# Optimization experiments

Hardware: AMD Instinct MI355X
Metric: run time of the kernel (lower is better)

Reference implementation:

```python
import jax, jax.numpy as jnp
import numpy as np

NUM_GROUPS = 8   # num_groups1, recursive_index=False path
NUM_HEADS = 8


def setup_inputs() -> dict:
    key = jax.random.key(0)
    k1, k2, k3 = jax.random.split(key, 3)
    B, C, H, W = 4, 256, 64, 64
    x = jax.random.normal(k1, (B, C, H, W), dtype=jnp.float32)
    w_qkv = jax.random.normal(k2, (3 * C, C), dtype=jnp.float32) * 0.02
    w_proj = jax.random.normal(k3, (C, C), dtype=jnp.float32) * 0.02
    b_proj = jnp.zeros((C,), dtype=jnp.float32)
    return {"x": x, "w_qkv": w_qkv, "w_proj": w_proj, "b_proj": b_proj}


def reference(x, w_qkv, w_proj, b_proj):
    B, C, H, W = x.shape
    N = H * W
    G = NUM_GROUPS
    nh = NUM_HEADS
    hd = C // nh
    M = N // G
    scale = hd ** -0.5

    # b c h w -> b (h w) c
    xf = x.reshape(B, C, N).transpose(0, 2, 1)  # [B, N, C]

    # qkv linear (no bias), then split into groups / heads
    qkv = (xf @ w_qkv.T).reshape(B, G, M, 3, nh, hd)
    qkv = jnp.transpose(qkv, (3, 0, 1, 4, 2, 5))  # [3, B, G, nh, M, hd]
    q, k, v = qkv[0], qkv[1], qkv[2]

    # grouped multi-head attention, manual softmax
    attn = jax.nn.softmax(jnp.einsum('bghmd,bghnd->bghmn', q, k) * scale, axis=-1)
    out = jnp.einsum('bghmn,bghnd->bghmd', attn, v)

    # [B,G,nh,M,hd] -> [B,G,M,C] -> [B,N,C]
    out = out.transpose(0, 1, 3, 2, 4).reshape(B, N, C)

    out = out @ w_proj.T + b_proj

    # b (h w) c -> b c h w
    return out.transpose(0, 2, 1).reshape(B, C, H, W)
```

## Files before the change

kernel.cpp:

```cpp
#include <hip/hip_runtime.h>
#include <hip/hip_bf16.h>

#define Bb 4
#define Cc 256
#define Nn 4096
#define Gg 8
#define NHh 8
#define HDd 32
#define Mm 512

typedef __bf16 bf16_t;
typedef __bf16 bf16x2 __attribute__((ext_vector_type(2)));
typedef __bf16 bf16x4 __attribute__((ext_vector_type(4)));
typedef __bf16 bf16x8 __attribute__((ext_vector_type(8)));
typedef float f32x4 __attribute__((ext_vector_type(4)));

#define LSCALE (0.17677669529663687f * 1.44269504088896340f)

__device__ __forceinline__ void load_lds16(const bf16_t* g, bf16_t* l) {
  __builtin_amdgcn_global_load_lds(
      (const __attribute__((address_space(1))) void*)g,
      (__attribute__((address_space(3))) void*)l, 16, 0, 0);
}

__global__ __launch_bounds__(256) void prep_kernel(
    const float* __restrict__ x, bf16_t* __restrict__ xT,
    const float* __restrict__ wqkv, const float* __restrict__ wproj,
    bf16_t* __restrict__ wq_b, bf16_t* __restrict__ wp_b) {
  int bid = blockIdx.x, tid = threadIdx.x;
  if (bid >= 1024) {
    int i = (bid - 1024) * 256 + tid;
    wq_b[i] = (bf16_t)wqkv[i];
    if (i < Cc * Cc) wp_b[i] = (bf16_t)wproj[i];
    return;
  }
  __shared__ float t[64][65];
  int b = bid >> 8, c0 = ((bid >> 6) & 3) * 64, n0 = (bid & 63) * 64;
  const float* xp = x + ((long long)b * Cc + c0) * Nn + n0;
#pragma unroll
  for (int it = 0; it < 4; ++it) {
    int idx = it * 256 + tid;
    int r = idx >> 4, col = (idx & 15) * 4;
    f32x4 v = *(const f32x4*)&xp[(long long)r * Nn + col];
    t[r][col] = v[0];
    t[r][col + 1] = v[1];
    t[r][col + 2] = v[2];
    t[r][col + 3] = v[3];
  }
  __syncthreads();
  bf16_t* op = xT + ((long long)b * Nn + n0) * Cc + c0;
#pragma unroll
  for (int it = 0; it < 2; ++it) {
    int idx = it * 256 + tid;
    int n = idx >> 3, cg = (idx & 7) * 8;
    bf16x8 w;
#pragma unroll
    for (int j = 0; j < 8; ++j) w[j] = (bf16_t)t[cg + j][n];
    *(bf16x8*)&op[(long long)n * Cc + cg] = w;
  }
}

__global__ __launch_bounds__(256, 4) void qkv_gemm_kernel(
    const bf16_t* __restrict__ xT, const bf16_t* __restrict__ wqb,
    bf16_t* __restrict__ Qh, bf16_t* __restrict__ Kh, bf16_t* __restrict__ Vh) {
  __shared__ bf16_t smem[20480];
  int bid = blockIdx.x;
  int m0 = (bid / 3) * 64;
  int n0 = (bid % 3) * 256;
  int tid = threadIdx.x, lane = tid & 63, wid = tid >> 6;
  int quad = lane >> 4, l16 = lane & 15;
  int wn = wid * 64;

  f32x4 acc[4][4];
#pragma unroll
  for (int i = 0; i < 4; ++i)
#pragma unroll
    for (int j = 0; j < 4; ++j) acc[i][j] = (f32x4){0.f, 0.f, 0.f, 0.f};

  int scol = (lane & 3) * 8;
  int arow = lane >> 2;
  auto stage = [&](int bufi, int k0) {
    load_lds16(&xT[(long long)(m0 + wid * 16 + arow) * Cc + k0 + scol],
               &smem[bufi * 2048 + wid * 512]);
#pragma unroll
    for (int r = 0; r < 4; ++r) {
      int ch = wid * 4 + r;
      load_lds16(&wqb[(long long)(n0 + ch * 16 + arow) * Cc + k0 + scol],
                 &smem[4096 + bufi * 8192 + ch * 512]);
    }
  };

  stage(0, 0);
  __syncthreads();
  for (int t = 0; t < 8; ++t) {
    if (t < 7) stage((t + 1) & 1, (t + 1) * 32);
    const bf16_t* Ap = &smem[(t & 1) * 2048];
    const bf16_t* Bp = &smem[4096 + (t & 1) * 8192];
    bf16x8 a[4], b[4];
#pragma unroll
    for (int i = 0; i < 4; ++i)
      a[i] = *(const bf16x8*)&Ap[(i * 16 + l16) * 32 + quad * 8];
#pragma unroll
    for (int j = 0; j < 4; ++j)
      b[j] = *(const bf16x8*)&Bp[(wn + j * 16 + l16) * 32 + quad * 8];
#pragma unroll
    for (int i = 0; i < 4; ++i)
#pragma unroll
      for (int j = 0; j < 4; ++j)
        acc[i][j] = __builtin_amdgcn_mfma_f32_16x16x32_bf16(a[i], b[j], acc[i][j], 0, 0, 0);
    __syncthreads();
  }

  if (n0 < 512) {
    const bool isQ = (n0 == 0);
    const float s = isQ ? LSCALE : 1.0f;
#pragma unroll
    for (int i = 0; i < 4; ++i)
#pragma unroll
      for (int j = 0; j < 4; ++j) {
        int f = wn + j * 16 + l16;
#pragma unroll
        for (int r = 0; r < 4; ++r) {
          int lm = i * 16 + quad * 4 + r;
          smem[lm * 268 + f] = (bf16_t)(acc[i][j][r] * s);
        }
      }
    __syncthreads();
    int lm = tid >> 2, d0 = (tid & 3) * 8;
    int row = m0 + lm;
    int bb = row >> 12, gg = (row >> 9) & 7, m = row & 511;
    bf16_t* dst = isQ ? Qh : Kh;
#pragma unroll
    for (int hh = 0; hh < 8; ++hh) {
      long long hb = (long long)((bb << 6) | (gg << 3) | hh) * (Mm * HDd);
      bf16x8 w = *(bf16x8*)&smem[lm * 268 + hh * 32 + d0];
      *(bf16x8*)&dst[hb + m * HDd + d0] = w;
    }
  } else {
#pragma unroll
    for (int i = 0; i < 4; ++i)
#pragma unroll
      for (int j = 0; j < 4; ++j) {
        int f = wn + j * 16 + l16;
#pragma unroll
        for (int r = 0; r < 4; ++r)
          smem[f * 72 + i * 16 + quad * 4 + r] = (bf16_t)acc[i][j][r];
      }
    __syncthreads();
    int bb = m0 >> 12, gg = (m0 >> 9) & 7, mb = m0 & 511;
#pragma unroll
    for (int it = 0; it < 8; ++it) {
      int idx = it * 256 + tid;
      int f = idx >> 3, seg = idx & 7;
      int hh = f >> 5, d = f & 31;
      long long hb = (long long)((bb << 6) | (gg << 3) | hh) * (Mm * HDd);
      bf16x8 w = *(bf16x8*)&smem[f * 72 + seg * 8];
      *(bf16x8*)&Vh[hb + (long long)d * Mm + mb + seg * 8] = w;
    }
  }
}

__global__ __launch_bounds__(256, 4) void attn_kernel(
    const bf16_t* __restrict__ Qh, const bf16_t* __restrict__ Kh,
    const bf16_t* __restrict__ Vh, bf16_t* __restrict__ Oa) {
  __shared__ bf16_t Ks[256 * 32];
  __shared__ bf16_t Vs[32 * 264];
  int gid = blockIdx.x;
  int ms = gid & 3, head = gid >> 2;
  int h = head & 7, g = (head >> 3) & 7, b = head >> 6;
  int tid = threadIdx.x, lane = tid & 63, wid = tid >> 6;
  int quad = lane >> 4, l16 = lane & 15;

  const bf16_t* Kg = Kh + (long long)head * (Mm * HDd);
  const bf16_t* Vg = Vh + (long long)head * (Mm * HDd);
  const bf16_t* Qg = Qh + (long long)head * (Mm * HDd) + (ms * 128 + wid * 32) * HDd;

  bf16x8 qa = *(const bf16x8*)&Qg[l16 * HDd + quad * 8];
  bf16x8 qb = *(const bf16x8*)&Qg[(16 + l16) * HDd + quad * 8];

  bf16x8 ones;
#pragma unroll
  for (int i = 0; i < 8; ++i) ones[i] = (bf16_t)1.0f;

  int rp0 = ((l16 >> 2) << 3) | (l16 & 3);
  const bf16_t* Kp0 = &Ks[rp0 * HDd + quad * 8];
  const bf16_t* Kp1 = Kp0 + 4 * HDd;
  const bf16_t* VsL = &Vs[l16 * 264 + quad * 8];
  const bf16_t* VsH = &Vs[(16 + l16) * 264 + quad * 8];
  const f32x4 zero = (f32x4){0.f, 0.f, 0.f, 0.f};

  f32x4 oLa = zero, oHa = zero, oLb = zero, oHb = zero;
  f32x4 ra = zero, rb = zero;

  auto inner = [&]() {
#pragma unroll
    for (int c = 0; c < 8; ++c) {
      int nb = c * 32;
      bf16x8 kf0 = *(const bf16x8*)&Kp0[nb * HDd];
      bf16x8 kf1 = *(const bf16x8*)&Kp1[nb * HDd];
      f32x4 sa0 = __builtin_amdgcn_mfma_f32_16x16x32_bf16(kf0, qa, zero, 0, 0, 0);
      f32x4 sa1 = __builtin_amdgcn_mfma_f32_16x16x32_bf16(kf1, qa, zero, 0, 0, 0);
      f32x4 sb0 = __builtin_amdgcn_mfma_f32_16x16x32_bf16(kf0, qb, zero, 0, 0, 0);
      f32x4 sb1 = __builtin_amdgcn_mfma_f32_16x16x32_bf16(kf1, qb, zero, 0, 0, 0);
      bf16x8 pa, pb;
#pragma unroll
      for (int r = 0; r < 4; ++r) {
        pa[r] = (bf16_t)__builtin_exp2f(sa0[r]);
        pa[4 + r] = (bf16_t)__builtin_exp2f(sa1[r]);
        pb[r] = (bf16_t)__builtin_exp2f(sb0[r]);
        pb[4 + r] = (bf16_t)__builtin_exp2f(sb1[r]);
      }
      bf16x8 vL = *(const bf16x8*)&VsL[nb];
      bf16x8 vH = *(const bf16x8*)&VsH[nb];
      oLa = __builtin_amdgcn_mfma_f32_16x16x32_bf16(vL, pa, oLa, 0, 0, 0);
      oHa = __builtin_amdgcn_mfma_f32_16x16x32_bf16(vH, pa, oHa, 0, 0, 0);
      oLb = __builtin_amdgcn_mfma_f32_16x16x32_bf16(vL, pb, oLb, 0, 0, 0);
      oHb = __builtin_amdgcn_mfma_f32_16x16x32_bf16(vH, pb, oHb, 0, 0, 0);
      ra = __builtin_amdgcn_mfma_f32_16x16x32_bf16(ones, pa, ra, 0, 0, 0);
      rb = __builtin_amdgcn_mfma_f32_16x16x32_bf16(ones, pb, rb, 0, 0, 0);
    }
  };

#pragma unroll
  for (int it = 0; it < 4; ++it) {
    int ch = wid * 4 + it;
    load_lds16(&Kg[ch * 512 + lane * 8], &Ks[ch * 512]);
  }
  bf16x8 vcur[4], vnxt[4];
#pragma unroll
  for (int i = 0; i < 4; ++i) {
    int idx = i * 256 + tid;
    int d = idx >> 5, c16 = idx & 31;
    vcur[i] = *(const bf16x8*)&Vg[d * Mm + c16 * 8];
    vnxt[i] = *(const bf16x8*)&Vg[d * Mm + 256 + c16 * 8];
  }
#pragma unroll
  for (int i = 0; i < 4; ++i) {
    int idx = i * 256 + tid;
    int d = idx >> 5, c16 = idx & 31;
    *(bf16x8*)&Vs[d * 264 + c16 * 8] = vcur[i];
  }
  __syncthreads();
  inner();
  __syncthreads();
#pragma unroll
  for (int it = 0; it < 4; ++it) {
    int ch = wid * 4 + it;
    load_lds16(&Kg[8192 + ch * 512 + lane * 8], &Ks[ch * 512]);
  }
#pragma unroll
  for (int i = 0; i < 4; ++i) {
    int idx = i * 256 + tid;
    int d = idx >> 5, c16 = idx & 31;
    *(bf16x8*)&Vs[d * 264 + c16 * 8] = vnxt[i];
  }
  __syncthreads();
  inner();

  float inva = 1.f / ra[0], invb = 1.f / rb[0];

  long long orowa =
      ((long long)(b * Nn + g * Mm + ms * 128 + wid * 32 + l16)) * Cc + h * HDd;
  long long orowb = orowa + 16 * Cc;
  bf16x4 wLa, wHa, wLb, wHb;
#pragma unroll
  for (int r = 0; r < 4; ++r) {
    wLa[r] = (bf16_t)(oLa[r] * inva);
    wHa[r] = (bf16_t)(oHa[r] * inva);
    wLb[r] = (bf16_t)(oLb[r] * invb);
    wHb[r] = (bf16_t)(oHb[r] * invb);
  }
  *(bf16x4*)&Oa[orowa + quad * 4] = wLa;
  *(bf16x4*)&Oa[orowa + 16 + quad * 4] = wHa;
  *(bf16x4*)&Oa[orowb + quad * 4] = wLb;
  *(bf16x4*)&Oa[orowb + 16 + quad * 4] = wHb;
}

__global__ __launch_bounds__(256, 4) void proj_kernel(
    const bf16_t* __restrict__ Wp, const bf16_t* __restrict__ Oa,
    float* __restrict__ out, const float* __restrict__ bias) {
  __shared__ bf16_t As[2][64 * 32];
  __shared__ bf16_t Bs[2][64 * 32];
  int tid = threadIdx.x, lane = tid & 63, wid = tid >> 6;
  int quad = lane >> 4, l16 = lane & 15;
  int z = blockIdx.z;
  const bf16_t* Bt = Oa + (long long)z * Nn * Cc;
  int m0 = blockIdx.y * 64, n0 = blockIdx.x * 64;

  f32x4 acc[4];
#pragma unroll
  for (int i = 0; i < 4; ++i) acc[i] = (f32x4){0.f, 0.f, 0.f, 0.f};

  int scol = (lane & 3) * 8;
  int arow = lane >> 2;
  auto stage = [&](int bufi, int k0) {
    load_lds16(&Wp[(long long)(m0 + wid * 16 + arow) * Cc + k0 + scol],
               &As[bufi][wid * 512]);
    load_lds16(&Bt[(long long)(n0 + wid * 16 + arow) * Cc + k0 + scol],
               &Bs[bufi][wid * 512]);
  };

  stage(0, 0);
  __syncthreads();
  for (int t = 0; t < 8; ++t) {
    if (t < 7) stage((t + 1) & 1, (t + 1) * 32);
    const bf16_t* Ap = As[t & 1];
    const bf16_t* Bp = Bs[t & 1];
    bf16x8 a[4], b;
#pragma unroll
    for (int i = 0; i < 4; ++i)
      a[i] = *(const bf16x8*)&Ap[(i * 16 + l16) * 32 + quad * 8];
    b = *(const bf16x8*)&Bp[(wid * 16 + l16) * 32 + quad * 8];
#pragma unroll
    for (int i = 0; i < 4; ++i)
      acc[i] = __builtin_amdgcn_mfma_f32_16x16x32_bf16(a[i], b, acc[i], 0, 0, 0);
    __syncthreads();
  }

#pragma unroll
  for (int i = 0; i < 4; ++i) {
    int col = n0 + wid * 16 + l16;
#pragma unroll
    for (int r = 0; r < 4; ++r) {
      int row = m0 + i * 16 + quad * 4 + r;
      out[(long long)z * (Cc * Nn) + (long long)row * Nn + col] =
          acc[i][r] + bias[row];
    }
  }
}

extern "C" void kernel_launch(void* const* d_in, const int* in_sizes, int n_in,
                              void* d_out, int out_size, void* d_ws, size_t ws_size,
                              hipStream_t stream) {
  (void)in_sizes; (void)n_in; (void)out_size; (void)ws_size;
  const float* x = (const float*)d_in[0];
  const float* w_qkv = (const float*)d_in[1];
  const float* w_proj = (const float*)d_in[2];
  const float* b_proj = (const float*)d_in[3];
  float* out = (float*)d_out;

  char* ws = (char*)d_ws;
  bf16_t* xT  = (bf16_t*)(ws);
  bf16_t* wqb = (bf16_t*)(ws + 8388608);
  bf16_t* wpb = (bf16_t*)(ws + 8781824);
  bf16_t* Qh  = (bf16_t*)(ws + 8912896);
  bf16_t* Kh  = (bf16_t*)(ws + 17301504);
  bf16_t* Vh  = (bf16_t*)(ws + 25690112);
  bf16_t* Oa  = (bf16_t*)(ws + 34078720);

  prep_kernel<<<1792, 256, 0, stream>>>(x, xT, w_qkv, w_proj, wqb, wpb);
  qkv_gemm_kernel<<<768, 256, 0, stream>>>(xT, wqb, Qh, Kh, Vh);
  attn_kernel<<<1024, 256, 0, stream>>>(Qh, Kh, Vh, Oa);
  proj_kernel<<<dim3(64, 4, 4), 256, 0, stream>>>(wpb, Oa, out, b_proj);
}
```

Measured before the change: 120.0 us.

## Stage full-K activation tile in LDS once, stream weights directly from global

```diff
diff --git a/kernel.cpp b/kernel.cpp
--- a/kernel.cpp
+++ b/kernel.cpp
@@ -63,7 +63,7 @@
 __global__ __launch_bounds__(256, 4) void qkv_gemm_kernel(
     const bf16_t* __restrict__ xT, const bf16_t* __restrict__ wqb,
     bf16_t* __restrict__ Qh, bf16_t* __restrict__ Kh, bf16_t* __restrict__ Vh) {
-  __shared__ bf16_t smem[20480];
+  __shared__ bf16_t smem[18432];
   int bid = blockIdx.x;
   int m0 = (bid / 3) * 64;
   int n0 = (bid % 3) * 256;
@@ -71,45 +71,43 @@
   int quad = lane >> 4, l16 = lane & 15;
   int wn = wid * 64;
 
+  {
+    int row = tid >> 2, seg = tid & 3;
+    const bf16_t* src = &xT[(long long)(m0 + row) * Cc + seg * 64];
+    bf16x8 tmp[8];
+#pragma unroll
+    for (int j = 0; j < 8; ++j) tmp[j] = *(const bf16x8*)&src[j * 8];
+#pragma unroll
+    for (int j = 0; j < 8; ++j)
+      *(bf16x8*)&smem[row * 266 + seg * 64 + j * 8] = tmp[j];
+  }
+
   f32x4 acc[4][4];
 #pragma unroll
   for (int i = 0; i < 4; ++i)
 #pragma unroll
     for (int j = 0; j < 4; ++j) acc[i][j] = (f32x4){0.f, 0.f, 0.f, 0.f};
 
-  int scol = (lane & 3) * 8;
-  int arow = lane >> 2;
-  auto stage = [&](int bufi, int k0) {
-    load_lds16(&xT[(long long)(m0 + wid * 16 + arow) * Cc + k0 + scol],
-               &smem[bufi * 2048 + wid * 512]);
-#pragma unroll
-    for (int r = 0; r < 4; ++r) {
-      int ch = wid * 4 + r;
-      load_lds16(&wqb[(long long)(n0 + ch * 16 + arow) * Cc + k0 + scol],
-                 &smem[4096 + bufi * 8192 + ch * 512]);
-    }
-  };
-
-  stage(0, 0);
-  __syncthreads();
+  __syncthreads();
+
+  const bf16_t* Bw = wqb + (long long)n0 * Cc;
+#pragma unroll
   for (int t = 0; t < 8; ++t) {
-    if (t < 7) stage((t + 1) & 1, (t + 1) * 32);
-    const bf16_t* Ap = &smem[(t & 1) * 2048];
-    const bf16_t* Bp = &smem[4096 + (t & 1) * 8192];
+    int k0 = t * 32;
     bf16x8 a[4], b[4];
 #pragma unroll
+    for (int j = 0; j < 4; ++j)
+      b[j] = *(const bf16x8*)&Bw[(long long)(wn + j * 16 + l16) * Cc + k0 + quad * 8];
+#pragma unroll
     for (int i = 0; i < 4; ++i)
-      a[i] = *(const bf16x8*)&Ap[(i * 16 + l16) * 32 + quad * 8];
-#pragma unroll
-    for (int j = 0; j < 4; ++j)
-      b[j] = *(const bf16x8*)&Bp[(wn + j * 16 + l16) * 32 + quad * 8];
+      a[i] = *(const bf16x8*)&smem[(i * 16 + l16) * 266 + k0 + quad * 8];
 #pragma unroll
     for (int i = 0; i < 4; ++i)
 #pragma unroll
       for (int j = 0; j < 4; ++j)
         acc[i][j] = __builtin_amdgcn_mfma_f32_16x16x32_bf16(a[i], b[j], acc[i][j], 0, 0, 0);
-    __syncthreads();
-  }
+  }
+  __syncthreads();
 
   if (n0 < 512) {
     const bool isQ = (n0 == 0);
@@ -279,52 +277,61 @@
 __global__ __launch_bounds__(256, 4) void proj_kernel(
     const bf16_t* __restrict__ Wp, const bf16_t* __restrict__ Oa,
     float* __restrict__ out, const float* __restrict__ bias) {
-  __shared__ bf16_t As[2][64 * 32];
-  __shared__ bf16_t Bs[2][64 * 32];
+  __shared__ bf16_t smem[64 * 266];
   int tid = threadIdx.x, lane = tid & 63, wid = tid >> 6;
   int quad = lane >> 4, l16 = lane & 15;
   int z = blockIdx.z;
+  int n0 = blockIdx.x * 64, i0 = blockIdx.y * 128;
   const bf16_t* Bt = Oa + (long long)z * Nn * Cc;
-  int m0 = blockIdx.y * 64, n0 = blockIdx.x * 64;
-
-  f32x4 acc[4];
-#pragma unroll
-  for (int i = 0; i < 4; ++i) acc[i] = (f32x4){0.f, 0.f, 0.f, 0.f};
-
-  int scol = (lane & 3) * 8;
-  int arow = lane >> 2;
-  auto stage = [&](int bufi, int k0) {
-    load_lds16(&Wp[(long long)(m0 + wid * 16 + arow) * Cc + k0 + scol],
-               &As[bufi][wid * 512]);
-    load_lds16(&Bt[(long long)(n0 + wid * 16 + arow) * Cc + k0 + scol],
-               &Bs[bufi][wid * 512]);
-  };
-
-  stage(0, 0);
-  __syncthreads();
+
+  {
+    int row = tid >> 2, seg = tid & 3;
+    const bf16_t* src = &Bt[(long long)(n0 + row) * Cc + seg * 64];
+    bf16x8 tmp[8];
+#pragma unroll
+    for (int j = 0; j < 8; ++j) tmp[j] = *(const bf16x8*)&src[j * 8];
+#pragma unroll
+    for (int j = 0; j < 8; ++j)
+      *(bf16x8*)&smem[row * 266 + seg * 64 + j * 8] = tmp[j];
+  }
+
+  f32x4 acc[2][4];
+#pragma unroll
+  for (int i = 0; i < 2; ++i)
+#pragma unroll
+    for (int j = 0; j < 4; ++j) acc[i][j] = (f32x4){0.f, 0.f, 0.f, 0.f};
+
+  __syncthreads();
+
+  int wm = i0 + wid * 32;
+#pragma unroll
   for (int t = 0; t < 8; ++t) {
-    if (t < 7) stage((t + 1) & 1, (t + 1) * 32);
-    const bf16_t* Ap = As[t & 1];
-    const bf16_t* Bp = Bs[t & 1];
-    bf16x8 a[4], b;
-#pragma unroll
-    for (int i = 0; i < 4; ++i)
-      a[i] = *(const bf16x8*)&Ap[(i * 16 + l16) * 32 + quad * 8];
-    b = *(const bf16x8*)&Bp[(wid * 16 + l16) * 32 + quad * 8];
-#pragma unroll
-    for (int i = 0; i < 4; ++i)
-      acc[i] = __builtin_amdgcn_mfma_f32_16x16x32_bf16(a[i], b, acc[i], 0, 0, 0);
-    __syncthreads();
-  }
-
-#pragma unroll
-  for (int i = 0; i < 4; ++i) {
-    int col = n0 + wid * 16 + l16;
-#pragma unroll
-    for (int r = 0; r < 4; ++r) {
-      int row = m0 + i * 16 + quad * 4 + r;
-      out[(long long)z * (Cc * Nn) + (long long)row * Nn + col] =
-          acc[i][r] + bias[row];
+    int k0 = t * 32;
+    bf16x8 a[2], b[4];
+#pragma unroll
+    for (int i = 0; i < 2; ++i)
+      a[i] = *(const bf16x8*)&Wp[(long long)(wm + i * 16 + l16) * Cc + k0 + quad * 8];
+#pragma unroll
+    for (int j = 0; j < 4; ++j)
+      b[j] = *(const bf16x8*)&smem[(j * 16 + l16) * 266 + k0 + quad * 8];
+#pragma unroll
+    for (int i = 0; i < 2; ++i)
+#pragma unroll
+      for (int j = 0; j < 4; ++j)
+        acc[i][j] = __builtin_amdgcn_mfma_f32_16x16x32_bf16(a[i], b[j], acc[i][j], 0, 0, 0);
+  }
+
+#pragma unroll
+  for (int i = 0; i < 2; ++i) {
+#pragma unroll
+    for (int j = 0; j < 4; ++j) {
+      int col = n0 + j * 16 + l16;
+#pragma unroll
+      for (int r = 0; r < 4; ++r) {
+        int row = wm + i * 16 + quad * 4 + r;
+        out[(long long)z * (Cc * Nn) + (long long)row * Nn + col] =
+            acc[i][j][r] + bias[row];
+      }
     }
   }
 }
@@ -351,5 +358,5 @@
   prep_kernel<<<1792, 256, 0, stream>>>(x, xT, w_qkv, w_proj, wqb, wpb);
   qkv_gemm_kernel<<<768, 256, 0, stream>>>(xT, wqb, Qh, Kh, Vh);
   attn_kernel<<<1024, 256, 0, stream>>>(Qh, Kh, Vh, Oa);
-  proj_kernel<<<dim3(64, 4, 4), 256, 0, stream>>>(wpb, Oa, out, b_proj);
-}
+  proj_kernel<<<dim3(64, 2, 4), 256, 0, stream>>>(wpb, Oa, out, b_proj);
+}
```

Result: slower. 128.2 us (+6.8%).
